# Optimization experiments

Measured on AMD Instinct MI355X. Metric: run time of the kernel, lower is better.

Reference implementation:

```python
import jax, jax.numpy as jnp
import numpy as np

DN = ('NCHW', 'OIHW', 'NCHW')

def _conv(x, w, b=None):
    # x: [P, C, H, W], w: [1, C, k, k] -> [P, 1, H, W] with SAME padding
    y = jax.lax.conv_general_dilated(x, w, (1, 1), 'SAME', dimension_numbers=DN)
    if b is not None:
        y = y + b[None, :, None, None]
    return y

def setup_inputs() -> dict:
    key = jax.random.key(0)
    ks = jax.random.split(key, 6)
    T, P, H, W = 36, 64, 128, 256
    K = 5
    inputs = jax.random.normal(ks[0], (T, P, H, W), dtype=jnp.float32)
    w_reset = 0.1 * jax.random.normal(ks[1], (1, 2, K, K), dtype=jnp.float32)
    b_reset = jnp.zeros((1,), dtype=jnp.float32)
    w_update = 0.1 * jax.random.normal(ks[2], (1, 2, K, K), dtype=jnp.float32)
    b_update = jnp.zeros((1,), dtype=jnp.float32)
    w_out = 0.1 * jax.random.normal(ks[3], (1, 2, K, K), dtype=jnp.float32)
    gam = jnp.ones((P,), dtype=jnp.float32)
    add_weights = 0.02 * jax.random.normal(ks[4], (P, H, W), dtype=jnp.float32)
    bias = jnp.zeros((H, W), dtype=jnp.float32)
    return {"inputs": inputs, "w_reset": w_reset, "b_reset": b_reset,
            "w_update": w_update, "b_update": b_update, "w_out": w_out,
            "gam": gam, "add_weights": add_weights, "bias": bias}

def reference(inputs, w_reset, b_reset, w_update, b_update, w_out, gam, add_weights, bias):
    # inputs: [T, P, H, W]; renormalize by per-plant scale gam
    x = gam[None, :, None, None] * inputs
    x = x[:, :, None]  # [T, P, 1, H, W] (channel dim = 1)
    h0 = jnp.zeros_like(x[0])  # [P, 1, H, W]

    def step(h, xt):
        stacked = jnp.concatenate([xt, h], axis=1)  # [P, 2, H, W]
        u = jax.nn.sigmoid(_conv(stacked, w_update, b_update))  # update gate
        r = jax.nn.sigmoid(_conv(stacked, w_reset, b_reset))    # reset gate
        c = _conv(jnp.concatenate([xt, r * h], axis=1), w_out)  # candidate (no bias, no act)
        h_new = h * (1.0 - u) + c * u
        return h_new, h_new

    _, states = jax.lax.scan(step, h0, x)  # [T, P, 1, H, W]
    s = states[:, :, 0]  # [T, P, H, W]
    # final layer (additive=False, rnn_act=None): tanh then per-plant spatial weights
    xs = jnp.tanh(s) * add_weights[None]
    out_y = xs.sum(axis=1) + bias[None]  # [T, H, W]
    return out_y, xs
```

## Files before the change

### kernel.cpp

```cpp
#include <hip/hip_runtime.h>

constexpr int T = 36, P = 64, H = 128, W = 256;
constexpr int HW  = H * W;
constexpr int PHW = P * HW;

constexpr int TILE_H = 32, TILE_W = 64;
constexpr int SXH = 40, SW = 76;
constexpr int SRH = 36, SRW = 76;

__device__ __forceinline__ float fast_sigmoid(float z) {
    float e = __expf(-z);
    return __builtin_amdgcn_rcpf(1.0f + e);
}
__device__ __forceinline__ float fast_tanh(float x) {
    float e = __expf(-2.0f * fabsf(x));
    float t = (1.0f - e) * __builtin_amdgcn_rcpf(1.0f + e);
    return copysignf(t, x);
}

__global__ __launch_bounds__(256, 4) void gru_step(
    const float* __restrict__ x_t,
    const float* __restrict__ gam,
    const float* __restrict__ h_prev,
    float* __restrict__ h_next,
    const float* __restrict__ w_update, const float* __restrict__ b_update,
    const float* __restrict__ w_reset,  const float* __restrict__ b_reset,
    const float* __restrict__ w_out,
    const float* __restrict__ add_w,
    float* __restrict__ xs_t)
{
    __shared__ __align__(16) float sx[SXH][SW];
    __shared__ __align__(16) float sh[SXH][SW];
    __shared__ __align__(16) float srh[SRH][SRW];

    const int tid = threadIdx.x;
    const int p   = blockIdx.z;
    const int by  = blockIdx.y * TILE_H;
    const int bx  = blockIdx.x * TILE_W;

    const float gamma = gam[p];
    const float* __restrict__ xin = x_t    + (size_t)p * HW;
    const float* __restrict__ hin = h_prev + (size_t)p * HW;

    for (int i = tid; i < SXH * 18; i += 256) {
        const int r  = i / 18;
        const int c4 = i - r * 18;
        const int gy = by + r - 4;
        const int gx = bx + 4 * c4 - 4;
        float4 xv = make_float4(0.f, 0.f, 0.f, 0.f);
        float4 hv = xv;
        if ((unsigned)gy < (unsigned)H && (unsigned)gx < (unsigned)W) {
            const int idx = gy * W + gx;
            xv = *(const float4*)&xin[idx];
            hv = *(const float4*)&hin[idx];
            xv.x *= gamma; xv.y *= gamma; xv.z *= gamma; xv.w *= gamma;
        }
        const int sc = 2 + 4 * c4;
        sx[r][sc] = xv.x; sx[r][sc+1] = xv.y; sx[r][sc+2] = xv.z; sx[r][sc+3] = xv.w;
        sh[r][sc] = hv.x; sh[r][sc+1] = hv.y; sh[r][sc+2] = hv.z; sh[r][sc+3] = hv.w;
    }
    if (tid < 160) {
        const int r = tid >> 2;
        const int c = tid & 3;
        const int col = (c < 2) ? c : 72 + c;
        sx[r][col] = 0.f;
        sh[r][col] = 0.f;
    }
    __syncthreads();

    if (tid < 162) {
        const int b = tid / 18;
        const int g = tid - b * 18;
        const int sr0 = 4 * b;
        const int scw = 4 * g;
        const float br = b_reset[0];
        float racc[4][4], hold[4][4];
        #pragma unroll
        for (int k = 0; k < 4; ++k)
            #pragma unroll
            for (int c = 0; c < 4; ++c) racc[k][c] = br;

        #pragma unroll
        for (int ir = 0; ir < 8; ++ir) {
            const float4 xa = *(const float4*)&sx[sr0 + ir][scw];
            const float4 xb = *(const float4*)&sx[sr0 + ir][scw + 4];
            const float4 ha = *(const float4*)&sh[sr0 + ir][scw];
            const float4 hb = *(const float4*)&sh[sr0 + ir][scw + 4];
            const float vx[8] = {xa.x, xa.y, xa.z, xa.w, xb.x, xb.y, xb.z, xb.w};
            const float vh[8] = {ha.x, ha.y, ha.z, ha.w, hb.x, hb.y, hb.z, hb.w};
            if (ir >= 2 && ir <= 5) {
                #pragma unroll
                for (int c = 0; c < 4; ++c) hold[ir - 2][c] = vh[c + 2];
            }
            #pragma unroll
            for (int k = 0; k < 4; ++k) {
                const int dy = ir - k;
                if (dy >= 0 && dy <= 4) {
                    #pragma unroll
                    for (int dx = 0; dx < 5; ++dx) {
                        const float wx = w_reset[dy * 5 + dx];
                        const float wh = w_reset[25 + dy * 5 + dx];
                        #pragma unroll
                        for (int c = 0; c < 4; ++c) {
                            racc[k][c] = fmaf(vx[c + dx], wx, racc[k][c]);
                            racc[k][c] = fmaf(vh[c + dx], wh, racc[k][c]);
                        }
                    }
                }
            }
        }
        #pragma unroll
        for (int k = 0; k < 4; ++k)
            #pragma unroll
            for (int c = 0; c < 4; ++c)
                srh[4 * b + k][scw + 2 + c] = fast_sigmoid(racc[k][c]) * hold[k][c];
    }
    __syncthreads();

    if (tid < 128) {
        const int rb = tid >> 4;
        const int cg = tid & 15;
        const int oy = 4 * rb;
        const int ox = 4 * cg;
        const float bu = b_update[0];

        float uacc[4][4], cacc[4][4], hold[4][4];
        #pragma unroll
        for (int k = 0; k < 4; ++k)
            #pragma unroll
            for (int c = 0; c < 4; ++c) { uacc[k][c] = bu; cacc[k][c] = 0.f; }

        #pragma unroll
        for (int ir = 0; ir < 8; ++ir) {
            const int sr = oy + 2 + ir;
            const float4 xa = *(const float4*)&sx[sr][ox + 4];
            const float4 xb = *(const float4*)&sx[sr][ox + 8];
            const float4 ha = *(const float4*)&sh[sr][ox + 4];
            const float4 hb = *(const float4*)&sh[sr][ox + 8];
            const float4 ra = *(const float4*)&srh[oy + ir][ox + 4];
            const float4 rb4 = *(const float4*)&srh[oy + ir][ox + 8];
            const float vx[8] = {xa.x, xa.y, xa.z, xa.w, xb.x, xb.y, xb.z, xb.w};
            const float vh[8] = {ha.x, ha.y, ha.z, ha.w, hb.x, hb.y, hb.z, hb.w};
            const float vr[8] = {ra.x, ra.y, ra.z, ra.w, rb4.x, rb4.y, rb4.z, rb4.w};
            if (ir >= 2 && ir <= 5) {
                #pragma unroll
                for (int c = 0; c < 4; ++c) hold[ir - 2][c] = vh[c + 2];
            }
            #pragma unroll
            for (int k = 0; k < 4; ++k) {
                const int dy = ir - k;
                if (dy >= 0 && dy <= 4) {
                    #pragma unroll
                    for (int dx = 0; dx < 5; ++dx) {
                        const float wux = w_update[dy * 5 + dx];
                        const float wuh = w_update[25 + dy * 5 + dx];
                        const float wox = w_out[dy * 5 + dx];
                        const float wor = w_out[25 + dy * 5 + dx];
                        #pragma unroll
                        for (int c = 0; c < 4; ++c) {
                            uacc[k][c] = fmaf(vx[c + dx], wux, uacc[k][c]);
                            uacc[k][c] = fmaf(vh[c + dx], wuh, uacc[k][c]);
                            cacc[k][c] = fmaf(vx[c + dx], wox, cacc[k][c]);
                            cacc[k][c] = fmaf(vr[c + dx], wor, cacc[k][c]);
                        }
                    }
                }
            }
        }

        const float* __restrict__ aw   = add_w  + (size_t)p * HW;
        float* __restrict__ hout = h_next + (size_t)p * HW;
        float* __restrict__ xso  = xs_t   + (size_t)p * HW;
        #pragma unroll
        for (int k = 0; k < 4; ++k) {
            const int gidx = (by + oy + k) * W + (bx + ox);
            const float4 aw4 = *(const float4*)&aw[gidx];
            const float awv[4] = {aw4.x, aw4.y, aw4.z, aw4.w};
            float hn[4], xv[4];
            #pragma unroll
            for (int c = 0; c < 4; ++c) {
                const float u = fast_sigmoid(uacc[k][c]);
                hn[c] = hold[k][c] + (cacc[k][c] - hold[k][c]) * u;
                xv[c] = fast_tanh(hn[c]) * awv[c];
            }
            *(float4*)&hout[gidx] = make_float4(hn[0], hn[1], hn[2], hn[3]);
            *(float4*)&xso[gidx]  = make_float4(xv[0], xv[1], xv[2], xv[3]);
        }
    }
}

__global__ __launch_bounds__(256) void reduce_out(
    const float* __restrict__ xs, const float* __restrict__ bias,
    float* __restrict__ out_y)
{
    const int i4  = blockIdx.x * 256 + threadIdx.x;
    const int t   = i4 / (HW / 4);
    const int yx4 = i4 - t * (HW / 4);
    const float4* __restrict__ src = (const float4*)(xs + (size_t)t * PHW) + yx4;
    const float4  b4 = ((const float4*)bias)[yx4];
    float a0[4] = {b4.x, b4.y, b4.z, b4.w};
    float a1[4] = {0.f, 0.f, 0.f, 0.f};
    #pragma unroll 8
    for (int p = 0; p < P; p += 2) {
        const float4 v0 = src[(size_t)p * (HW / 4)];
        const float4 v1 = src[(size_t)(p + 1) * (HW / 4)];
        a0[0] += v0.x; a0[1] += v0.y; a0[2] += v0.z; a0[3] += v0.w;
        a1[0] += v1.x; a1[1] += v1.y; a1[2] += v1.z; a1[3] += v1.w;
    }
    ((float4*)out_y)[i4] = make_float4(a0[0] + a1[0], a0[1] + a1[1],
                                       a0[2] + a1[2], a0[3] + a1[3]);
}

extern "C" void kernel_launch(void* const* d_in, const int* in_sizes, int n_in,
                              void* d_out, int out_size, void* d_ws, size_t ws_size,
                              hipStream_t stream) {
    const float* inputs   = (const float*)d_in[0];
    const float* w_reset  = (const float*)d_in[1];
    const float* b_reset  = (const float*)d_in[2];
    const float* w_update = (const float*)d_in[3];
    const float* b_update = (const float*)d_in[4];
    const float* w_out    = (const float*)d_in[5];
    const float* gam      = (const float*)d_in[6];
    const float* add_w    = (const float*)d_in[7];
    const float* bias     = (const float*)d_in[8];

    float* out_y = (float*)d_out;
    float* xs    = out_y + (size_t)T * HW;

    float* h0 = (float*)d_ws;
    float* h1 = h0 + (size_t)PHW;

    hipMemsetAsync(h0, 0, (size_t)PHW * sizeof(float), stream);

    dim3 grid(W / TILE_W, H / TILE_H, P);
    for (int t = 0; t < T; ++t) {
        const float* hp = (t & 1) ? h1 : h0;
        float*       hn = (t & 1) ? h0 : h1;
        gru_step<<<grid, 256, 0, stream>>>(
            inputs + (size_t)t * PHW, gam, hp, hn,
            w_update, b_update, w_reset, b_reset, w_out,
            add_w, xs + (size_t)t * PHW);
    }

    const int nout4 = T * HW / 4;
    reduce_out<<<nout4 / 256, 256, 0, stream>>>(xs, bias, out_y);
}
```

Measured before the change: 885.5 us.

## Fuse all GRU timesteps into one persistent kernel with neighbor halo exchange

Replaces the 36 per-timestep kernel launches with a single persistent kernel of 512 blocks. Each block owns a 16-row band of one plant and keeps its hidden state in LDS across steps. Bands exchange only the 4-row halos through a global buffer, using per-block flags and spin waits on adjacent neighbors. This removes launch overhead and the full global read/write of h each step, and the next input is loaded before the sync. The cost is that all 512 blocks must be co-resident, and the timeout fallback silently drops synchronization if they are not, which risks incorrect results.

```diff
diff --git a/kernel.cpp b/kernel.cpp
--- a/kernel.cpp
+++ b/kernel.cpp
@@ -4,9 +4,14 @@
 constexpr int HW  = H * W;
 constexpr int PHW = P * HW;
 
-constexpr int TILE_H = 32, TILE_W = 64;
-constexpr int SXH = 40, SW = 76;
-constexpr int SRH = 36, SRW = 76;
+constexpr int TH  = 16;
+constexpr int NB  = 8;
+constexpr int NBLK = P * NB;
+constexpr int SR = 24, SC = 268;
+constexpr int RR = 20;
+
+constexpr long long TMO_ARRIVE = 3000000;
+constexpr long long TMO_STEP   = 1000000;
 
 __device__ __forceinline__ float fast_sigmoid(float z) {
     float e = __expf(-z);
@@ -18,174 +23,282 @@
     return copysignf(t, x);
 }
 
-__global__ __launch_bounds__(256, 4) void gru_step(
-    const float* __restrict__ x_t,
-    const float* __restrict__ gam,
-    const float* __restrict__ h_prev,
-    float* __restrict__ h_next,
+__device__ __forceinline__ void lds_store4(float* d, float4 v) {
+    *(float2*)d       = make_float2(v.x, v.y);
+    *(float2*)(d + 2) = make_float2(v.z, v.w);
+}
+
+__global__ __launch_bounds__(256, 2) void gru_all(
+    const float* __restrict__ inputs, const float* __restrict__ gam,
     const float* __restrict__ w_update, const float* __restrict__ b_update,
     const float* __restrict__ w_reset,  const float* __restrict__ b_reset,
-    const float* __restrict__ w_out,
-    const float* __restrict__ add_w,
-    float* __restrict__ xs_t)
+    const float* __restrict__ w_out,    const float* __restrict__ add_w,
+    float* __restrict__ xs, float* __restrict__ hhalo, int* __restrict__ flags)
 {
-    __shared__ __align__(16) float sx[SXH][SW];
-    __shared__ __align__(16) float sh[SXH][SW];
-    __shared__ __align__(16) float srh[SRH][SRW];
-
-    const int tid = threadIdx.x;
-    const int p   = blockIdx.z;
-    const int by  = blockIdx.y * TILE_H;
-    const int bx  = blockIdx.x * TILE_W;
+    __shared__ __align__(16) float sx[SR][SC];
+    __shared__ __align__(16) float sh[SR][SC];
+    __shared__ __align__(16) float srh[RR][SC];
+
+    const int tid  = threadIdx.x;
+    const int bid  = blockIdx.x;
+    const int p    = bid >> 3;
+    const int band = bid & 7;
+    const int y0   = band * TH;
 
     const float gamma = gam[p];
-    const float* __restrict__ xin = x_t    + (size_t)p * HW;
-    const float* __restrict__ hin = h_prev + (size_t)p * HW;
-
-    for (int i = tid; i < SXH * 18; i += 256) {
-        const int r  = i / 18;
-        const int c4 = i - r * 18;
-        const int gy = by + r - 4;
-        const int gx = bx + 4 * c4 - 4;
-        float4 xv = make_float4(0.f, 0.f, 0.f, 0.f);
-        float4 hv = xv;
-        if ((unsigned)gy < (unsigned)H && (unsigned)gx < (unsigned)W) {
-            const int idx = gy * W + gx;
-            xv = *(const float4*)&xin[idx];
-            hv = *(const float4*)&hin[idx];
-            xv.x *= gamma; xv.y *= gamma; xv.z *= gamma; xv.w *= gamma;
-        }
-        const int sc = 2 + 4 * c4;
-        sx[r][sc] = xv.x; sx[r][sc+1] = xv.y; sx[r][sc+2] = xv.z; sx[r][sc+3] = xv.w;
-        sh[r][sc] = hv.x; sh[r][sc+1] = hv.y; sh[r][sc+2] = hv.z; sh[r][sc+3] = hv.w;
-    }
-    if (tid < 160) {
-        const int r = tid >> 2;
-        const int c = tid & 3;
-        const int col = (c < 2) ? c : 72 + c;
-        sx[r][col] = 0.f;
-        sh[r][col] = 0.f;
+    const float bu = b_update[0];
+    const float br = b_reset[0];
+
+    const int cg = tid & 63, rbb = tid >> 6;
+    const int ox = 4 * cg,   oy  = 4 * rbb;
+
+    int nowait = 0;
+    if (tid == 0) {
+        __hip_atomic_fetch_add(&flags[NBLK], 1, __ATOMIC_ACQ_REL, __HIP_MEMORY_SCOPE_AGENT);
+        const long long t0 = (long long)__builtin_amdgcn_s_memrealtime();
+        while (__hip_atomic_load(&flags[NBLK], __ATOMIC_ACQUIRE, __HIP_MEMORY_SCOPE_AGENT) < NBLK) {
+            __builtin_amdgcn_s_sleep(16);
+            if ((long long)__builtin_amdgcn_s_memrealtime() - t0 > TMO_ARRIVE) { nowait = 1; break; }
+        }
+    }
+
+    float4 aw4[4];
+    #pragma unroll
+    for (int k = 0; k < 4; ++k)
+        aw4[k] = *(const float4*)&add_w[(size_t)p * HW + (y0 + oy + k) * W + ox];
+
+    for (int s = tid; s < SR * SC; s += 256) {
+        (&sx[0][0])[s] = 0.f;
+        (&sh[0][0])[s] = 0.f;
     }
     __syncthreads();
-
-    if (tid < 162) {
-        const int b = tid / 18;
-        const int g = tid - b * 18;
-        const int sr0 = 4 * b;
-        const int scw = 4 * g;
-        const float br = b_reset[0];
-        float racc[4][4], hold[4][4];
+    {
+        const float* xt = inputs + (size_t)p * HW;
+        for (int s = tid; s < SR * 64; s += 256) {
+            const int r = s >> 6, c4 = s & 63;
+            const int gy = y0 + r - 4;
+            if ((unsigned)gy < (unsigned)H) {
+                float4 v = *(const float4*)&xt[gy * W + 4 * c4];
+                v.x *= gamma; v.y *= gamma; v.z *= gamma; v.w *= gamma;
+                lds_store4(&sx[r][6 + 4 * c4], v);
+            }
+        }
+    }
+    __syncthreads();
+
+    #pragma unroll 1
+    for (int t = 0; t < T; ++t) {
+        for (int s = tid; s < 330; s += 256) {
+            const int b5 = s / 66;
+            const int g  = s - b5 * 66;
+            const int r0 = 4 * b5;
+            const int c0 = 4 * g;
+            float racc[4][4], hold[4][4];
+            #pragma unroll
+            for (int k = 0; k < 4; ++k)
+                #pragma unroll
+                for (int c = 0; c < 4; ++c) racc[k][c] = br;
+            #pragma unroll
+            for (int ir = 0; ir < 8; ++ir) {
+                const float4 xa = *(const float4*)&sx[r0 + ir][c0];
+                const float4 xb = *(const float4*)&sx[r0 + ir][c0 + 4];
+                const float4 ha = *(const float4*)&sh[r0 + ir][c0];
+                const float4 hb = *(const float4*)&sh[r0 + ir][c0 + 4];
+                const float vx[8] = {xa.x, xa.y, xa.z, xa.w, xb.x, xb.y, xb.z, xb.w};
+                const float vh[8] = {ha.x, ha.y, ha.z, ha.w, hb.x, hb.y, hb.z, hb.w};
+                if (ir >= 2 && ir <= 5) {
+                    #pragma unroll
+                    for (int c = 0; c < 4; ++c) hold[ir - 2][c] = vh[c + 2];
+                }
+                #pragma unroll
+                for (int k = 0; k < 4; ++k) {
+                    const int dy = ir - k;
+                    if (dy >= 0 && dy <= 4) {
+                        #pragma unroll
+                        for (int dx = 0; dx < 5; ++dx) {
+                            const float wx = w_reset[dy * 5 + dx];
+                            const float wh = w_reset[25 + dy * 5 + dx];
+                            #pragma unroll
+                            for (int c = 0; c < 4; ++c) {
+                                racc[k][c] = fmaf(vx[c + dx], wx, racc[k][c]);
+                                racc[k][c] = fmaf(vh[c + dx], wh, racc[k][c]);
+                            }
+                        }
+                    }
+                }
+            }
+            #pragma unroll
+            for (int k = 0; k < 4; ++k) {
+                float4 v;
+                v.x = fast_sigmoid(racc[k][0]) * hold[k][0];
+                v.y = fast_sigmoid(racc[k][1]) * hold[k][1];
+                v.z = fast_sigmoid(racc[k][2]) * hold[k][2];
+                v.w = fast_sigmoid(racc[k][3]) * hold[k][3];
+                lds_store4(&srh[r0 + k][c0 + 2], v);
+            }
+        }
+        __syncthreads();
+
+        float4 hn4[4];
+        {
+            float uacc[4][4], cacc[4][4], hold[4][4];
+            #pragma unroll
+            for (int k = 0; k < 4; ++k)
+                #pragma unroll
+                for (int c = 0; c < 4; ++c) { uacc[k][c] = bu; cacc[k][c] = 0.f; }
+            #pragma unroll
+            for (int ir = 0; ir < 8; ++ir) {
+                const int sr = oy + 2 + ir;
+                const float4 xa = *(const float4*)&sx[sr][ox + 4];
+                const float4 xb = *(const float4*)&sx[sr][ox + 8];
+                const float4 ha = *(const float4*)&sh[sr][ox + 4];
+                const float4 hb = *(const float4*)&sh[sr][ox + 8];
+                const float4 ra = *(const float4*)&srh[oy + ir][ox + 4];
+                const float4 rb = *(const float4*)&srh[oy + ir][ox + 8];
+                const float vx[8] = {xa.x, xa.y, xa.z, xa.w, xb.x, xb.y, xb.z, xb.w};
+                const float vh[8] = {ha.x, ha.y, ha.z, ha.w, hb.x, hb.y, hb.z, hb.w};
+                const float vr[8] = {ra.x, ra.y, ra.z, ra.w, rb.x, rb.y, rb.z, rb.w};
+                if (ir >= 2 && ir <= 5) {
+                    #pragma unroll
+                    for (int c = 0; c < 4; ++c) hold[ir - 2][c] = vh[c + 2];
+                }
+                #pragma unroll
+                for (int k = 0; k < 4; ++k) {
+                    const int dy = ir - k;
+                    if (dy >= 0 && dy <= 4) {
+                        #pragma unroll
+                        for (int dx = 0; dx < 5; ++dx) {
+                            const float wux = w_update[dy * 5 + dx];
+                            const float wuh = w_update[25 + dy * 5 + dx];
+                            const float wox = w_out[dy * 5 + dx];
+                            const float wor = w_out[25 + dy * 5 + dx];
+                            #pragma unroll
+                            for (int c = 0; c < 4; ++c) {
+                                uacc[k][c] = fmaf(vx[c + dx], wux, uacc[k][c]);
+                                uacc[k][c] = fmaf(vh[c + dx], wuh, uacc[k][c]);
+                                cacc[k][c] = fmaf(vx[c + dx], wox, cacc[k][c]);
+                                cacc[k][c] = fmaf(vr[c + dx], wor, cacc[k][c]);
+                            }
+                        }
+                    }
+                }
+            }
+            #pragma unroll
+            for (int k = 0; k < 4; ++k) {
+                float hn[4];
+                #pragma unroll
+                for (int c = 0; c < 4; ++c) {
+                    const float u = fast_sigmoid(uacc[k][c]);
+                    hn[c] = hold[k][c] + (cacc[k][c] - hold[k][c]) * u;
+                }
+                hn4[k] = make_float4(hn[0], hn[1], hn[2], hn[3]);
+            }
+        }
+        __syncthreads();
+
         #pragma unroll
         for (int k = 0; k < 4; ++k)
-            #pragma unroll
-            for (int c = 0; c < 4; ++c) racc[k][c] = br;
-
-        #pragma unroll
-        for (int ir = 0; ir < 8; ++ir) {
-            const float4 xa = *(const float4*)&sx[sr0 + ir][scw];
-            const float4 xb = *(const float4*)&sx[sr0 + ir][scw + 4];
-            const float4 ha = *(const float4*)&sh[sr0 + ir][scw];
-            const float4 hb = *(const float4*)&sh[sr0 + ir][scw + 4];
-            const float vx[8] = {xa.x, xa.y, xa.z, xa.w, xb.x, xb.y, xb.z, xb.w};
-            const float vh[8] = {ha.x, ha.y, ha.z, ha.w, hb.x, hb.y, hb.z, hb.w};
-            if (ir >= 2 && ir <= 5) {
-                #pragma unroll
-                for (int c = 0; c < 4; ++c) hold[ir - 2][c] = vh[c + 2];
-            }
+            lds_store4(&sh[4 + oy + k][6 + ox], hn4[k]);
+
+        {
+            float* hb = hhalo + (size_t)(t & 1) * (NBLK * 2048) + (size_t)bid * 2048;
+            if (rbb == 0) {
+                #pragma unroll
+                for (int k = 0; k < 4; ++k) {
+                    float* d = &hb[k * 256 + ox];
+                    __hip_atomic_store(&d[0], hn4[k].x, __ATOMIC_RELAXED, __HIP_MEMORY_SCOPE_AGENT);
+                    __hip_atomic_store(&d[1], hn4[k].y, __ATOMIC_RELAXED, __HIP_MEMORY_SCOPE_AGENT);
+                    __hip_atomic_store(&d[2], hn4[k].z, __ATOMIC_RELAXED, __HIP_MEMORY_SCOPE_AGENT);
+                    __hip_atomic_store(&d[3], hn4[k].w, __ATOMIC_RELAXED, __HIP_MEMORY_SCOPE_AGENT);
+                }
+            }
+            if (rbb == 3) {
+                #pragma unroll
+                for (int k = 0; k < 4; ++k) {
+                    float* d = &hb[(4 + k) * 256 + ox];
+                    __hip_atomic_store(&d[0], hn4[k].x, __ATOMIC_RELAXED, __HIP_MEMORY_SCOPE_AGENT);
+                    __hip_atomic_store(&d[1], hn4[k].y, __ATOMIC_RELAXED, __HIP_MEMORY_SCOPE_AGENT);
+                    __hip_atomic_store(&d[2], hn4[k].z, __ATOMIC_RELAXED, __HIP_MEMORY_SCOPE_AGENT);
+                    __hip_atomic_store(&d[3], hn4[k].w, __ATOMIC_RELAXED, __HIP_MEMORY_SCOPE_AGENT);
+                }
+            }
+        }
+        {
+            float* xso = xs + (size_t)t * PHW + (size_t)p * HW;
             #pragma unroll
             for (int k = 0; k < 4; ++k) {
-                const int dy = ir - k;
-                if (dy >= 0 && dy <= 4) {
-                    #pragma unroll
-                    for (int dx = 0; dx < 5; ++dx) {
-                        const float wx = w_reset[dy * 5 + dx];
-                        const float wh = w_reset[25 + dy * 5 + dx];
-                        #pragma unroll
-                        for (int c = 0; c < 4; ++c) {
-                            racc[k][c] = fmaf(vx[c + dx], wx, racc[k][c]);
-                            racc[k][c] = fmaf(vh[c + dx], wh, racc[k][c]);
-                        }
-                    }
-                }
-            }
-        }
-        #pragma unroll
-        for (int k = 0; k < 4; ++k)
-            #pragma unroll
-            for (int c = 0; c < 4; ++c)
-                srh[4 * b + k][scw + 2 + c] = fast_sigmoid(racc[k][c]) * hold[k][c];
-    }
-    __syncthreads();
-
-    if (tid < 128) {
-        const int rb = tid >> 4;
-        const int cg = tid & 15;
-        const int oy = 4 * rb;
-        const int ox = 4 * cg;
-        const float bu = b_update[0];
-
-        float uacc[4][4], cacc[4][4], hold[4][4];
-        #pragma unroll
-        for (int k = 0; k < 4; ++k)
-            #pragma unroll
-            for (int c = 0; c < 4; ++c) { uacc[k][c] = bu; cacc[k][c] = 0.f; }
-
-        #pragma unroll
-        for (int ir = 0; ir < 8; ++ir) {
-            const int sr = oy + 2 + ir;
-            const float4 xa = *(const float4*)&sx[sr][ox + 4];
-            const float4 xb = *(const float4*)&sx[sr][ox + 8];
-            const float4 ha = *(const float4*)&sh[sr][ox + 4];
-            const float4 hb = *(const float4*)&sh[sr][ox + 8];
-            const float4 ra = *(const float4*)&srh[oy + ir][ox + 4];
-            const float4 rb4 = *(const float4*)&srh[oy + ir][ox + 8];
-            const float vx[8] = {xa.x, xa.y, xa.z, xa.w, xb.x, xb.y, xb.z, xb.w};
-            const float vh[8] = {ha.x, ha.y, ha.z, ha.w, hb.x, hb.y, hb.z, hb.w};
-            const float vr[8] = {ra.x, ra.y, ra.z, ra.w, rb4.x, rb4.y, rb4.z, rb4.w};
-            if (ir >= 2 && ir <= 5) {
-                #pragma unroll
-                for (int c = 0; c < 4; ++c) hold[ir - 2][c] = vh[c + 2];
-            }
-            #pragma unroll
-            for (int k = 0; k < 4; ++k) {
-                const int dy = ir - k;
-                if (dy >= 0 && dy <= 4) {
-                    #pragma unroll
-                    for (int dx = 0; dx < 5; ++dx) {
-                        const float wux = w_update[dy * 5 + dx];
-                        const float wuh = w_update[25 + dy * 5 + dx];
-                        const float wox = w_out[dy * 5 + dx];
-                        const float wor = w_out[25 + dy * 5 + dx];
-                        #pragma unroll
-                        for (int c = 0; c < 4; ++c) {
-                            uacc[k][c] = fmaf(vx[c + dx], wux, uacc[k][c]);
-                            uacc[k][c] = fmaf(vh[c + dx], wuh, uacc[k][c]);
-                            cacc[k][c] = fmaf(vx[c + dx], wox, cacc[k][c]);
-                            cacc[k][c] = fmaf(vr[c + dx], wor, cacc[k][c]);
-                        }
-                    }
-                }
-            }
-        }
-
-        const float* __restrict__ aw   = add_w  + (size_t)p * HW;
-        float* __restrict__ hout = h_next + (size_t)p * HW;
-        float* __restrict__ xso  = xs_t   + (size_t)p * HW;
-        #pragma unroll
-        for (int k = 0; k < 4; ++k) {
-            const int gidx = (by + oy + k) * W + (bx + ox);
-            const float4 aw4 = *(const float4*)&aw[gidx];
-            const float awv[4] = {aw4.x, aw4.y, aw4.z, aw4.w};
-            float hn[4], xv[4];
-            #pragma unroll
-            for (int c = 0; c < 4; ++c) {
-                const float u = fast_sigmoid(uacc[k][c]);
-                hn[c] = hold[k][c] + (cacc[k][c] - hold[k][c]) * u;
-                xv[c] = fast_tanh(hn[c]) * awv[c];
-            }
-            *(float4*)&hout[gidx] = make_float4(hn[0], hn[1], hn[2], hn[3]);
-            *(float4*)&xso[gidx]  = make_float4(xv[0], xv[1], xv[2], xv[3]);
-        }
+                float4 v;
+                v.x = fast_tanh(hn4[k].x) * aw4[k].x;
+                v.y = fast_tanh(hn4[k].y) * aw4[k].y;
+                v.z = fast_tanh(hn4[k].z) * aw4[k].z;
+                v.w = fast_tanh(hn4[k].w) * aw4[k].w;
+                *(float4*)&xso[(y0 + oy + k) * W + ox] = v;
+            }
+        }
+        if (t + 1 < T) {
+            const float* xt = inputs + (size_t)(t + 1) * PHW + (size_t)p * HW;
+            for (int s = tid; s < SR * 64; s += 256) {
+                const int r = s >> 6, c4 = s & 63;
+                const int gy = y0 + r - 4;
+                if ((unsigned)gy < (unsigned)H) {
+                    float4 v = *(const float4*)&xt[gy * W + 4 * c4];
+                    v.x *= gamma; v.y *= gamma; v.z *= gamma; v.w *= gamma;
+                    lds_store4(&sx[r][6 + 4 * c4], v);
+                }
+            }
+        }
+
+        if (t + 1 >= T) break;
+
+        __syncthreads();
+
+        if (tid == 0) {
+            __threadfence();
+            __hip_atomic_store(&flags[bid], t + 1, __ATOMIC_RELEASE, __HIP_MEMORY_SCOPE_AGENT);
+            if (!nowait) {
+                const long long t0 = (long long)__builtin_amdgcn_s_memrealtime();
+                if (band > 0)
+                    while (__hip_atomic_load(&flags[bid - 1], __ATOMIC_ACQUIRE, __HIP_MEMORY_SCOPE_AGENT) < t + 1) {
+                        __builtin_amdgcn_s_sleep(2);
+                        if ((long long)__builtin_amdgcn_s_memrealtime() - t0 > TMO_STEP) { nowait = 1; break; }
+                    }
+                if (band < 7 && !nowait)
+                    while (__hip_atomic_load(&flags[bid + 1], __ATOMIC_ACQUIRE, __HIP_MEMORY_SCOPE_AGENT) < t + 1) {
+                        __builtin_amdgcn_s_sleep(2);
+                        if ((long long)__builtin_amdgcn_s_memrealtime() - t0 > TMO_STEP) { nowait = 1; break; }
+                    }
+            }
+        }
+        __syncthreads();
+
+        {
+            float* hb0 = hhalo + (size_t)(t & 1) * (NBLK * 2048);
+            for (int s = tid; s < 512; s += 256) {
+                const int r = s >> 6, c4 = s & 63;
+                if (r < 4) {
+                    if (band > 0) {
+                        float* src = &hb0[(size_t)(bid - 1) * 2048 + (4 + r) * 256 + 4 * c4];
+                        float4 v;
+                        v.x = __hip_atomic_load(&src[0], __ATOMIC_RELAXED, __HIP_MEMORY_SCOPE_AGENT);
+                        v.y = __hip_atomic_load(&src[1], __ATOMIC_RELAXED, __HIP_MEMORY_SCOPE_AGENT);
+                        v.z = __hip_atomic_load(&src[2], __ATOMIC_RELAXED, __HIP_MEMORY_SCOPE_AGENT);
+                        v.w = __hip_atomic_load(&src[3], __ATOMIC_RELAXED, __HIP_MEMORY_SCOPE_AGENT);
+                        lds_store4(&sh[r][6 + 4 * c4], v);
+                    }
+                } else {
+                    if (band < 7) {
+                        float* src = &hb0[(size_t)(bid + 1) * 2048 + (r - 4) * 256 + 4 * c4];
+                        float4 v;
+                        v.x = __hip_atomic_load(&src[0], __ATOMIC_RELAXED, __HIP_MEMORY_SCOPE_AGENT);
+                        v.y = __hip_atomic_load(&src[1], __ATOMIC_RELAXED, __HIP_MEMORY_SCOPE_AGENT);
+                        v.z = __hip_atomic_load(&src[2], __ATOMIC_RELAXED, __HIP_MEMORY_SCOPE_AGENT);
+                        v.w = __hip_atomic_load(&src[3], __ATOMIC_RELAXED, __HIP_MEMORY_SCOPE_AGENT);
+                        lds_store4(&sh[16 + r][6 + 4 * c4], v);
+                    }
+                }
+            }
+        }
+        __syncthreads();
     }
 }
 
@@ -227,20 +340,14 @@
     float* out_y = (float*)d_out;
     float* xs    = out_y + (size_t)T * HW;
 
-    float* h0 = (float*)d_ws;
-    float* h1 = h0 + (size_t)PHW;
-
-    hipMemsetAsync(h0, 0, (size_t)PHW * sizeof(float), stream);
-
-    dim3 grid(W / TILE_W, H / TILE_H, P);
-    for (int t = 0; t < T; ++t) {
-        const float* hp = (t & 1) ? h1 : h0;
-        float*       hn = (t & 1) ? h0 : h1;
-        gru_step<<<grid, 256, 0, stream>>>(
-            inputs + (size_t)t * PHW, gam, hp, hn,
-            w_update, b_update, w_reset, b_reset, w_out,
-            add_w, xs + (size_t)t * PHW);
-    }
+    float* hhalo = (float*)d_ws;
+    int*   flags = (int*)((char*)d_ws + (size_t)2 * NBLK * 2048 * sizeof(float));
+
+    hipMemsetAsync(flags, 0, (NBLK + 1) * sizeof(int), stream);
+
+    gru_all<<<dim3(NBLK), dim3(256), 0, stream>>>(
+        inputs, gam, w_update, b_update, w_reset, b_reset, w_out, add_w,
+        xs, hhalo, flags);
 
     const int nout4 = T * HW / 4;
     reduce_out<<<nout4 / 256, 256, 0, stream>>>(xs, bias, out_y);
```

Measured after the change: 2.031 ms. +129.4%, slower.
